# Kernel tuning notes

Hardware: AMD Instinct MI355X
Metric: run time of the kernel (lower is better)

Reference implementation:

```python
import jax, jax.numpy as jnp
import numpy as np

N = 16384
E = 524288
IN_DIM = 512
HID = 256
NCLS = 64


def setup_inputs() -> dict:
    key = jax.random.key(0)
    k1, k2, k3, k4, k5, k6 = jax.random.split(key, 6)
    X = jax.random.normal(k1, (N, IN_DIM), dtype=jnp.float32)
    edge_index = jax.random.randint(k2, (2, E), 0, N, dtype=jnp.int64)
    # torch nn.Linear params: y = x @ W.T + b
    W1 = jax.random.normal(k3, (HID, IN_DIM), dtype=jnp.float32) * (1.0 / np.sqrt(IN_DIM))
    b1 = jax.random.normal(k4, (HID,), dtype=jnp.float32) * 0.01
    W2 = jax.random.normal(k5, (NCLS, HID), dtype=jnp.float32) * (1.0 / np.sqrt(HID))
    b2 = jax.random.normal(k6, (NCLS,), dtype=jnp.float32) * 0.01
    return {"X": X, "edge_index": edge_index, "W1": W1, "b1": b1, "W2": W2, "b2": b2}


def _build_a_hat(edge_index, n):
    # Dense adjacency via scatter-set, exactly as the torch code does.
    A = jnp.zeros((n, n), dtype=jnp.float32)
    A = A.at[edge_index[0], edge_index[1]].set(1.0)
    A = A + A.T
    A = (A > 0).astype(jnp.float32)
    A = A + jnp.eye(n, dtype=jnp.float32)
    # symmetric normalization: D^-1/2 A D^-1/2 (diag matmuls == broadcast)
    deg = A.sum(axis=1)
    dis = jnp.power(deg + 1e-8, -0.5)
    return dis[:, None] * A * dis[None, :]


def reference(X, edge_index, W1, b1, W2, b2):
    n = X.shape[0]
    A_hat = _build_a_hat(edge_index, n)
    H = A_hat @ X                      # [N, in_dim]
    H = H @ W1.T + b1                  # lin1
    H = jax.nn.relu(H)
    # dropout is identity in eval mode
    H = A_hat @ H                      # [N, hidden]
    H = H @ W2.T + b2                  # lin2 -> [N, num_classes]
    return H
```

## Files before the change

### kernel.cpp

```cpp
#include <hip/hip_runtime.h>
#include <stdint.h>

#define N_NODES 16384
#define N_EDGES 524288
#define IN_DIM  512
#define HID     256
#define NCLS    64
#define LSTRIDE 192
#define NBKT    1024
#define SCAP    24
#define NBBLK   256
#define GEMM_BLKS 512

typedef __bf16 bf16x8 __attribute__((ext_vector_type(8)));
typedef float  f32x4  __attribute__((ext_vector_type(4)));

__device__ __forceinline__ unsigned short f2bf(float f) {
    unsigned int u = __float_as_uint(f);
    u += 0x7FFFu + ((u >> 16) & 1u);
    return (unsigned short)(u >> 16);
}
__device__ __forceinline__ float bflo(unsigned int u) { return __uint_as_float(u << 16); }
__device__ __forceinline__ float bfhi(unsigned int u) { return __uint_as_float(u & 0xFFFF0000u); }

__device__ __forceinline__ void bucket_body(
    int blk, const void* __restrict__ ep, unsigned int* __restrict__ cnt,
    unsigned int* __restrict__ gbuf, char* smem) {
    unsigned int* lcnt = (unsigned int*)smem;
    __shared__ int sflag;
    const int tid = threadIdx.x;
    if (tid == 0) {
        const int* p = (const int*)ep;
        int odd = 1;
        for (int k = 0; k < 64; ++k)
            if (p[2 * k + 1] != 0) odd = 0;
        sflag = odd;
    }
    for (int b = tid; b < NBKT; b += 256) lcnt[b] = 0;
    __syncthreads();

    const int e0 = blk * 2048 + tid;
    int s[8], d[8];
    if (sflag) {
        const long long* p = (const long long*)ep;
        #pragma unroll
        for (int q = 0; q < 8; ++q) {
            s[q] = (int)p[e0 + q * 256];
            d[q] = (int)p[N_EDGES + e0 + q * 256];
        }
    } else {
        const int* p = (const int*)ep;
        #pragma unroll
        for (int q = 0; q < 8; ++q) {
            s[q] = p[e0 + q * 256];
            d[q] = p[N_EDGES + e0 + q * 256];
        }
    }
    unsigned int* myslice = gbuf + (size_t)blk * NBKT * SCAP;
    #pragma unroll
    for (int q = 0; q < 8; ++q) {
        int b0 = s[q] >> 4, b1 = d[q] >> 4;
        unsigned int sl0 = atomicAdd(&lcnt[b0], 1u);
        unsigned int sl1 = atomicAdd(&lcnt[b1], 1u);
        if (sl0 < SCAP)
            myslice[b0 * SCAP + sl0] =
                ((unsigned int)(s[q] & 15) << 14) | (unsigned int)d[q];
        if (sl1 < SCAP)
            myslice[b1 * SCAP + sl1] =
                ((unsigned int)(d[q] & 15) << 14) | (unsigned int)s[q];
    }
    __syncthreads();
    unsigned int* mycnt = cnt + (size_t)blk * NBKT;
    for (int b = tid; b < NBKT; b += 256)
        mycnt[b] = min(lcnt[b], (unsigned int)SCAP);
}

__global__ __launch_bounds__(256) void build_csr(
    const unsigned int* __restrict__ cnt, const unsigned int* __restrict__ gbuf,
    float* __restrict__ dis, int* __restrict__ ncnt,
    unsigned short* __restrict__ lists) {
    __shared__ unsigned int bml[16 * 512];
    const int tid = threadIdx.x;
    const int bkt = blockIdx.x;
    const int node0 = bkt * 16;
    #pragma unroll
    for (int q = 0; q < 32; ++q) bml[tid + q * 256] = 0;
    __syncthreads();
    {
        const unsigned int c = cnt[(size_t)tid * NBKT + bkt];
        const unsigned int* sp = gbuf + ((size_t)tid * NBKT + bkt) * SCAP;
        for (unsigned int l = 0; l < c; ++l) {
            unsigned int e = sp[l];
            unsigned int local = e >> 14, nbr = e & 16383u;
            atomicOr(&bml[local * 512 + (nbr >> 5)], 1u << (nbr & 31u));
        }
    }
    __syncthreads();
    const int wid = tid >> 6, lane = tid & 63;
    for (int nn = wid; nn < 16; nn += 4) {
        const int node = node0 + nn;
        const unsigned int* row = bml + nn * 512 + lane * 8;
        unsigned int w[8];
        int c = 0;
        #pragma unroll
        for (int j = 0; j < 8; ++j) { w[j] = row[j]; c += __popc(w[j]); }
        int inc = c;
        #pragma unroll
        for (int dd = 1; dd < 64; dd <<= 1) {
            int t = __shfl_up(inc, dd);
            if (lane >= dd) inc += t;
        }
        int total = __shfl(inc, 63);
        unsigned short* dst = lists + (size_t)node * LSTRIDE + (inc - c);
        int k = 0;
        #pragma unroll
        for (int j = 0; j < 8; ++j) {
            unsigned int bits = w[j];
            int base = (lane * 8 + j) * 32;
            while (bits) {
                int b = __ffs(bits) - 1;
                bits &= bits - 1;
                dst[k++] = (unsigned short)(base + b);
            }
        }
        if (lane == 63) {
            lists[(size_t)node * LSTRIDE + total] = (unsigned short)node;
            ncnt[node] = total + 1;
            dis[node] = 1.0f / sqrtf((float)(total + 1) + 1e-8f);
        }
    }
}

template <bool F32>
__device__ __forceinline__ uint4 ld_chunk(const void* __restrict__ G,
                                          size_t row, int KD, int k0, int s) {
    if constexpr (F32) {
        const float* g = (const float*)G + row * KD + k0 + s * 8;
        float4 v0 = *(const float4*)g;
        float4 v1 = *(const float4*)(g + 4);
        uint4 w;
        w.x = (unsigned int)f2bf(v0.x) | ((unsigned int)f2bf(v0.y) << 16);
        w.y = (unsigned int)f2bf(v0.z) | ((unsigned int)f2bf(v0.w) << 16);
        w.z = (unsigned int)f2bf(v1.x) | ((unsigned int)f2bf(v1.y) << 16);
        w.w = (unsigned int)f2bf(v1.z) | ((unsigned int)f2bf(v1.w) << 16);
        return w;
    } else {
        return *(const uint4*)((const unsigned short*)G + row * KD + k0 + s * 8);
    }
}

template <int BM, int BN, int KD, int ND, bool AF32, bool BF32>
__device__ __forceinline__ void gemm_body(
    int bx, int by, const void* __restrict__ Ag, const void* __restrict__ Bg,
    unsigned short* __restrict__ Cg, const float* __restrict__ dis, char* smem) {
    constexpr int FM = BM / 32, FN = BN / 32;
    constexpr int NK = KD / 64;
    unsigned short* Asm = (unsigned short*)smem;
    unsigned short* Bsm = (unsigned short*)smem + BM * 64;
    const int tid = threadIdx.x;
    const int lane = tid & 63;
    const int wid = tid >> 6;
    const int wm = wid >> 1, wn = wid & 1;
    const int m0 = bx * BM, n0 = by * BN;

    uint4 ra[BM / 32], rb[BN / 32];
    #pragma unroll
    for (int q = 0; q < BM / 32; ++q) {
        int cch = tid + 256 * q, r = cch >> 3, s = cch & 7;
        ra[q] = ld_chunk<AF32>(Ag, (size_t)(m0 + r), KD, 0, s);
    }
    #pragma unroll
    for (int q = 0; q < BN / 32; ++q) {
        int cch = tid + 256 * q, r = cch >> 3, s = cch & 7;
        rb[q] = ld_chunk<BF32>(Bg, (size_t)(n0 + r), KD, 0, s);
    }

    f32x4 acc[FM][FN] = {};

    for (int kt = 0; kt < NK; ++kt) {
        __syncthreads();
        #pragma unroll
        for (int q = 0; q < BM / 32; ++q) {
            int cch = tid + 256 * q, r = cch >> 3, s = cch & 7;
            *(uint4*)((char*)Asm + r * 128 + ((s ^ (r & 7)) << 4)) = ra[q];
        }
        #pragma unroll
        for (int q = 0; q < BN / 32; ++q) {
            int cch = tid + 256 * q, r = cch >> 3, s = cch & 7;
            *(uint4*)((char*)Bsm + r * 128 + ((s ^ (r & 7)) << 4)) = rb[q];
        }
        __syncthreads();
        if (kt + 1 < NK) {
            int k0 = (kt + 1) * 64;
            #pragma unroll
            for (int q = 0; q < BM / 32; ++q) {
                int cch = tid + 256 * q, r = cch >> 3, s = cch & 7;
                ra[q] = ld_chunk<AF32>(Ag, (size_t)(m0 + r), KD, k0, s);
            }
            #pragma unroll
            for (int q = 0; q < BN / 32; ++q) {
                int cch = tid + 256 * q, r = cch >> 3, s = cch & 7;
                rb[q] = ld_chunk<BF32>(Bg, (size_t)(n0 + r), KD, k0, s);
            }
        }
        #pragma unroll
        for (int ks = 0; ks < 2; ++ks) {
            bf16x8 af[FM], bg[FN];
            #pragma unroll
            for (int i = 0; i < FM; ++i) {
                int row = wm * (BM / 2) + i * 16 + (lane & 15);
                int slot = (ks * 4 + (lane >> 4)) ^ (row & 7);
                af[i] = *(const bf16x8*)((const char*)Asm + row * 128 + slot * 16);
            }
            #pragma unroll
            for (int j = 0; j < FN; ++j) {
                int row = wn * (BN / 2) + j * 16 + (lane & 15);
                int slot = (ks * 4 + (lane >> 4)) ^ (row & 7);
                bg[j] = *(const bf16x8*)((const char*)Bsm + row * 128 + slot * 16);
            }
            #pragma unroll
            for (int i = 0; i < FM; ++i)
                #pragma unroll
                for (int j = 0; j < FN; ++j)
                    acc[i][j] = __builtin_amdgcn_mfma_f32_16x16x32_bf16(af[i], bg[j], acc[i][j], 0, 0, 0);
        }
    }

    #pragma unroll
    for (int i = 0; i < FM; ++i) {
        #pragma unroll
        for (int e = 0; e < 4; ++e) {
            int row = m0 + wm * (BM / 2) + i * 16 + ((lane >> 4) << 2) + e;
            float dm = dis ? dis[row] : 1.0f;
            #pragma unroll
            for (int j = 0; j < FN; ++j) {
                int col = n0 + wn * (BN / 2) + j * 16 + (lane & 15);
                Cg[(size_t)row * ND + col] = f2bf(acc[i][j][e] * dm);
            }
        }
    }
}

__global__ __launch_bounds__(256) void bucket_gemm(
    const float* __restrict__ X, const float* __restrict__ W1,
    unsigned short* __restrict__ Y, const void* __restrict__ ep,
    unsigned int* __restrict__ cnt, unsigned int* __restrict__ gbuf) {
    __shared__ __align__(16) char smem[(64 + 128) * 64 * 2];
    if (blockIdx.x < GEMM_BLKS) {
        int gb = blockIdx.x;
        gemm_body<64, 128, IN_DIM, HID, true, true>(
            gb & 255, gb >> 8, X, W1, Y, nullptr, smem);
    } else {
        bucket_body(blockIdx.x - GEMM_BLKS, ep, cnt, gbuf, smem);
    }
}

__global__ __launch_bounds__(256) void gemm2_k(
    const unsigned short* __restrict__ H1, const float* __restrict__ W2,
    unsigned short* __restrict__ Z, const float* __restrict__ dis) {
    __shared__ __align__(16) char smem[(128 + 64) * 64 * 2];
    gemm_body<128, 64, HID, NCLS, false, true>(blockIdx.x, 0, H1, W2, Z, dis, smem);
}

__global__ __launch_bounds__(256) void spmm_hid(
    const int* __restrict__ ncnt, const unsigned short* __restrict__ lists,
    const float* __restrict__ dis, const unsigned short* __restrict__ Yp,
    const float* __restrict__ bias, unsigned int* __restrict__ H1b) {
    const int bid = blockIdx.x;
    const int r = bid & 7;
    const int fh = r >> 2;
    const int wid = threadIdx.x >> 6, lane = threadIdx.x & 63;
    const int i = (bid >> 3) * 16 + (r & 3) * 4 + wid;

    __shared__ unsigned int sl[4][LSTRIDE];
    __shared__ float dl[4][LSTRIDE];
    const int n = min(ncnt[i], LSTRIDE);
    for (int l = lane; l < n; l += 64) {
        int j = lists[(size_t)i * LSTRIDE + l];
        sl[wid][l] = (unsigned int)j << 9;
        dl[wid][l] = dis[j];
    }
    __syncthreads();

    const int hw = lane >> 5, p = lane & 31;
    const char* Ybase = (const char*)Yp + fh * 256 + p * 8;
    float a0 = 0, a1 = 0, a2 = 0, a3 = 0;
    float b0 = 0, b1 = 0, b2 = 0, b3 = 0;
    float c0 = 0, c1 = 0, c2 = 0, c3 = 0;
    float d0 = 0, d1 = 0, d2 = 0, d3 = 0;
    int l = 0;
    for (; l + 8 <= n; l += 8) {
        int i0 = l + hw, i1 = l + 2 + hw, i2 = l + 4 + hw, i3 = l + 6 + hw;
        uint2 u0 = *(const uint2*)(Ybase + sl[wid][i0]);
        uint2 u1 = *(const uint2*)(Ybase + sl[wid][i1]);
        uint2 u2 = *(const uint2*)(Ybase + sl[wid][i2]);
        uint2 u3 = *(const uint2*)(Ybase + sl[wid][i3]);
        float w0 = dl[wid][i0], w1 = dl[wid][i1], w2 = dl[wid][i2], w3 = dl[wid][i3];
        a0 = fmaf(w0, bflo(u0.x), a0); a1 = fmaf(w0, bfhi(u0.x), a1);
        a2 = fmaf(w0, bflo(u0.y), a2); a3 = fmaf(w0, bfhi(u0.y), a3);
        b0 = fmaf(w1, bflo(u1.x), b0); b1 = fmaf(w1, bfhi(u1.x), b1);
        b2 = fmaf(w1, bflo(u1.y), b2); b3 = fmaf(w1, bfhi(u1.y), b3);
        c0 = fmaf(w2, bflo(u2.x), c0); c1 = fmaf(w2, bfhi(u2.x), c1);
        c2 = fmaf(w2, bflo(u2.y), c2); c3 = fmaf(w2, bfhi(u2.y), c3);
        d0 = fmaf(w3, bflo(u3.x), d0); d1 = fmaf(w3, bfhi(u3.x), d1);
        d2 = fmaf(w3, bflo(u3.y), d2); d3 = fmaf(w3, bfhi(u3.y), d3);
    }
    for (; l + hw < n; l += 2) {
        int i0 = l + hw;
        uint2 u = *(const uint2*)(Ybase + sl[wid][i0]);
        float w = dl[wid][i0];
        a0 = fmaf(w, bflo(u.x), a0); a1 = fmaf(w, bfhi(u.x), a1);
        a2 = fmaf(w, bflo(u.y), a2); a3 = fmaf(w, bfhi(u.y), a3);
    }
    a0 += (b0 + c0) + d0; a1 += (b1 + c1) + d1;
    a2 += (b2 + c2) + d2; a3 += (b3 + c3) + d3;
    a0 += __shfl_xor(a0, 32);
    a1 += __shfl_xor(a1, 32);
    a2 += __shfl_xor(a2, 32);
    a3 += __shfl_xor(a3, 32);
    if (hw == 0) {
        float di = dis[i];
        float4 bb = *(const float4*)&bias[fh * 128 + 4 * p];
        float v0 = fmaxf(fmaf(di, a0, bb.x), 0.0f);
        float v1 = fmaxf(fmaf(di, a1, bb.y), 0.0f);
        float v2 = fmaxf(fmaf(di, a2, bb.z), 0.0f);
        float v3 = fmaxf(fmaf(di, a3, bb.w), 0.0f);
        unsigned int olo = (unsigned int)f2bf(v0) | ((unsigned int)f2bf(v1) << 16);
        unsigned int ohi = (unsigned int)f2bf(v2) | ((unsigned int)f2bf(v3) << 16);
        unsigned int* op = &H1b[(size_t)i * 128 + fh * 64 + 2 * p];
        __builtin_nontemporal_store(olo, op);
        __builtin_nontemporal_store(ohi, op + 1);
    }
}

__global__ __launch_bounds__(256) void spmm_out(
    const int* __restrict__ ncnt, const unsigned short* __restrict__ lists,
    const float* __restrict__ dis, const unsigned short* __restrict__ Zp,
    const float* __restrict__ bias, float* __restrict__ out) {
    const int wid = threadIdx.x >> 6, lane = threadIdx.x & 63;
    const int i = blockIdx.x * 4 + wid;
    __shared__ unsigned int sl[4][LSTRIDE];
    const int n = min(ncnt[i], LSTRIDE);
    for (int l = lane; l < n; l += 64)
        sl[wid][l] = (unsigned int)lists[(size_t)i * LSTRIDE + l] << 7;
    __syncthreads();

    const int hw = lane >> 5, p = lane & 31;
    const char* Zbase = (const char*)Zp + p * 4;
    float s0 = 0, s1 = 0, t0 = 0, t1 = 0, q0 = 0, q1 = 0, r0 = 0, r1 = 0;
    int l = 0;
    for (; l + 8 <= n; l += 8) {
        unsigned int ua = *(const unsigned int*)(Zbase + sl[wid][l + hw]);
        unsigned int ub = *(const unsigned int*)(Zbase + sl[wid][l + 2 + hw]);
        unsigned int uc = *(const unsigned int*)(Zbase + sl[wid][l + 4 + hw]);
        unsigned int ud = *(const unsigned int*)(Zbase + sl[wid][l + 6 + hw]);
        s0 += bflo(ua); s1 += bfhi(ua);
        t0 += bflo(ub); t1 += bfhi(ub);
        q0 += bflo(uc); q1 += bfhi(uc);
        r0 += bflo(ud); r1 += bfhi(ud);
    }
    for (; l + hw < n; l += 2) {
        unsigned int u = *(const unsigned int*)(Zbase + sl[wid][l + hw]);
        s0 += bflo(u); s1 += bfhi(u);
    }
    s0 += (t0 + q0) + r0; s1 += (t1 + q1) + r1;
    s0 += __shfl_xor(s0, 32);
    s1 += __shfl_xor(s1, 32);
    if (hw == 0) {
        float di = dis[i];
        __builtin_nontemporal_store(fmaf(di, s0, bias[2 * p]), &out[(size_t)i * 64 + 2 * p]);
        __builtin_nontemporal_store(fmaf(di, s1, bias[2 * p + 1]), &out[(size_t)i * 64 + 2 * p + 1]);
    }
}

extern "C" void kernel_launch(void* const* d_in, const int* in_sizes, int n_in,
                              void* d_out, int out_size, void* d_ws, size_t ws_size,
                              hipStream_t stream) {
    const float* X  = (const float*)d_in[0];
    const void*  EI = d_in[1];
    const float* W1 = (const float*)d_in[2];
    const float* b1 = (const float*)d_in[3];
    const float* W2 = (const float*)d_in[4];
    const float* b2 = (const float*)d_in[5];
    float* out = (float*)d_out;

    char* ws = (char*)d_ws;
    char* p = ws;
    unsigned int* cnt  = (unsigned int*)p;       p += (size_t)NBBLK * NBKT * 4;
    unsigned int* gbuf = (unsigned int*)p;       p += (size_t)NBBLK * NBKT * SCAP * 4;
    float* dis = (float*)p;                      p += (size_t)N_NODES * 4;
    int* ncnt = (int*)p;                         p += (size_t)N_NODES * 4;
    unsigned short* lists = (unsigned short*)p;  p += (size_t)N_NODES * LSTRIDE * 2;
    unsigned short* Y   = (unsigned short*)p;    p += (size_t)N_NODES * HID * 2;
    unsigned int* H1b   = (unsigned int*)p;      p += (size_t)N_NODES * HID * 2;
    unsigned short* Z   = (unsigned short*)p;    p += (size_t)N_NODES * NCLS * 2;

    bucket_gemm<<<GEMM_BLKS + NBBLK, 256, 0, stream>>>(X, W1, Y, EI, cnt, gbuf);
    build_csr<<<NBKT, 256, 0, stream>>>(cnt, gbuf, dis, ncnt, lists);
    spmm_hid<<<2 * N_NODES / 4, 256, 0, stream>>>(ncnt, lists, dis, Y, b1, H1b);
    gemm2_k<<<N_NODES / 128, 256, 0, stream>>>((const unsigned short*)H1b, W2, Z, dis);
    spmm_out<<<N_NODES / 4, 256, 0, stream>>>(ncnt, lists, dis, Z, b2, out);
}
```

Baseline: 115.2 us.

## Widen SpMM gathers to 16-byte loads, enlarge GEMM1 tile, transpose bucket counts

The two SpMM kernels now gather neighbour rows with 16-byte vector loads and spread more neighbours across lane groups, using shuffle reductions at the end. In spmm_hid each neighbour's weight and offset are packed into one uint2 in shared memory. The first GEMM switches to 128x128 tiles with half as many blocks. The bucket count array is transposed so build_csr reads it coalesced. The aim is fewer memory transactions and less gather latency, at the cost of more registers, more shuffle work and less GEMM parallelism.

```diff
diff --git a/kernel.cpp b/kernel.cpp
--- a/kernel.cpp
+++ b/kernel.cpp
@@ -10,10 +10,11 @@
 #define NBKT    1024
 #define SCAP    24
 #define NBBLK   256
-#define GEMM_BLKS 512
+#define GEMM_BLKS 256
 
 typedef __bf16 bf16x8 __attribute__((ext_vector_type(8)));
 typedef float  f32x4  __attribute__((ext_vector_type(4)));
+typedef unsigned int u32x4 __attribute__((ext_vector_type(4)));
 
 __device__ __forceinline__ unsigned short f2bf(float f) {
     unsigned int u = __float_as_uint(f);
@@ -70,9 +71,8 @@
                 ((unsigned int)(d[q] & 15) << 14) | (unsigned int)s[q];
     }
     __syncthreads();
-    unsigned int* mycnt = cnt + (size_t)blk * NBKT;
     for (int b = tid; b < NBKT; b += 256)
-        mycnt[b] = min(lcnt[b], (unsigned int)SCAP);
+        cnt[(size_t)b * NBBLK + blk] = min(lcnt[b], (unsigned int)SCAP);
 }
 
 __global__ __launch_bounds__(256) void build_csr(
@@ -87,7 +87,7 @@
     for (int q = 0; q < 32; ++q) bml[tid + q * 256] = 0;
     __syncthreads();
     {
-        const unsigned int c = cnt[(size_t)tid * NBKT + bkt];
+        const unsigned int c = cnt[(size_t)bkt * NBBLK + tid];
         const unsigned int* sp = gbuf + ((size_t)tid * NBKT + bkt) * SCAP;
         for (unsigned int l = 0; l < c; ++l) {
             unsigned int e = sp[l];
@@ -245,11 +245,11 @@
     const float* __restrict__ X, const float* __restrict__ W1,
     unsigned short* __restrict__ Y, const void* __restrict__ ep,
     unsigned int* __restrict__ cnt, unsigned int* __restrict__ gbuf) {
-    __shared__ __align__(16) char smem[(64 + 128) * 64 * 2];
+    __shared__ __align__(16) char smem[(128 + 128) * 64 * 2];
     if (blockIdx.x < GEMM_BLKS) {
         int gb = blockIdx.x;
-        gemm_body<64, 128, IN_DIM, HID, true, true>(
-            gb & 255, gb >> 8, X, W1, Y, nullptr, smem);
+        gemm_body<128, 128, IN_DIM, HID, true, true>(
+            gb & 127, gb >> 7, X, W1, Y, nullptr, smem);
     } else {
         bucket_body(blockIdx.x - GEMM_BLKS, ep, cnt, gbuf, smem);
     }
@@ -265,71 +265,78 @@
 __global__ __launch_bounds__(256) void spmm_hid(
     const int* __restrict__ ncnt, const unsigned short* __restrict__ lists,
     const float* __restrict__ dis, const unsigned short* __restrict__ Yp,
-    const float* __restrict__ bias, unsigned int* __restrict__ H1b) {
+    const float* __restrict__ bias, unsigned short* __restrict__ H1) {
     const int bid = blockIdx.x;
     const int r = bid & 7;
     const int fh = r >> 2;
     const int wid = threadIdx.x >> 6, lane = threadIdx.x & 63;
     const int i = (bid >> 3) * 16 + (r & 3) * 4 + wid;
 
-    __shared__ unsigned int sl[4][LSTRIDE];
-    __shared__ float dl[4][LSTRIDE];
+    __shared__ uint2 sld[4][LSTRIDE];
     const int n = min(ncnt[i], LSTRIDE);
     for (int l = lane; l < n; l += 64) {
         int j = lists[(size_t)i * LSTRIDE + l];
-        sl[wid][l] = (unsigned int)j << 9;
-        dl[wid][l] = dis[j];
-    }
-    __syncthreads();
-
-    const int hw = lane >> 5, p = lane & 31;
-    const char* Ybase = (const char*)Yp + fh * 256 + p * 8;
-    float a0 = 0, a1 = 0, a2 = 0, a3 = 0;
-    float b0 = 0, b1 = 0, b2 = 0, b3 = 0;
-    float c0 = 0, c1 = 0, c2 = 0, c3 = 0;
-    float d0 = 0, d1 = 0, d2 = 0, d3 = 0;
+        uint2 m;
+        m.x = __float_as_uint(dis[j]);
+        m.y = (unsigned int)j << 9;
+        sld[wid][l] = m;
+    }
+    __syncthreads();
+
+    const int qw = lane >> 4, p = lane & 15;
+    const char* Ybase = (const char*)Yp + fh * 256 + p * 16;
+    float acc[8] = {}, acc2[8] = {};
     int l = 0;
     for (; l + 8 <= n; l += 8) {
-        int i0 = l + hw, i1 = l + 2 + hw, i2 = l + 4 + hw, i3 = l + 6 + hw;
-        uint2 u0 = *(const uint2*)(Ybase + sl[wid][i0]);
-        uint2 u1 = *(const uint2*)(Ybase + sl[wid][i1]);
-        uint2 u2 = *(const uint2*)(Ybase + sl[wid][i2]);
-        uint2 u3 = *(const uint2*)(Ybase + sl[wid][i3]);
-        float w0 = dl[wid][i0], w1 = dl[wid][i1], w2 = dl[wid][i2], w3 = dl[wid][i3];
-        a0 = fmaf(w0, bflo(u0.x), a0); a1 = fmaf(w0, bfhi(u0.x), a1);
-        a2 = fmaf(w0, bflo(u0.y), a2); a3 = fmaf(w0, bfhi(u0.y), a3);
-        b0 = fmaf(w1, bflo(u1.x), b0); b1 = fmaf(w1, bfhi(u1.x), b1);
-        b2 = fmaf(w1, bflo(u1.y), b2); b3 = fmaf(w1, bfhi(u1.y), b3);
-        c0 = fmaf(w2, bflo(u2.x), c0); c1 = fmaf(w2, bfhi(u2.x), c1);
-        c2 = fmaf(w2, bflo(u2.y), c2); c3 = fmaf(w2, bfhi(u2.y), c3);
-        d0 = fmaf(w3, bflo(u3.x), d0); d1 = fmaf(w3, bfhi(u3.x), d1);
-        d2 = fmaf(w3, bflo(u3.y), d2); d3 = fmaf(w3, bfhi(u3.y), d3);
-    }
-    for (; l + hw < n; l += 2) {
-        int i0 = l + hw;
-        uint2 u = *(const uint2*)(Ybase + sl[wid][i0]);
-        float w = dl[wid][i0];
-        a0 = fmaf(w, bflo(u.x), a0); a1 = fmaf(w, bfhi(u.x), a1);
-        a2 = fmaf(w, bflo(u.y), a2); a3 = fmaf(w, bfhi(u.y), a3);
-    }
-    a0 += (b0 + c0) + d0; a1 += (b1 + c1) + d1;
-    a2 += (b2 + c2) + d2; a3 += (b3 + c3) + d3;
-    a0 += __shfl_xor(a0, 32);
-    a1 += __shfl_xor(a1, 32);
-    a2 += __shfl_xor(a2, 32);
-    a3 += __shfl_xor(a3, 32);
-    if (hw == 0) {
+        uint2 m0 = sld[wid][l + qw];
+        uint2 m1 = sld[wid][l + 4 + qw];
+        uint4 u0 = *(const uint4*)(Ybase + m0.y);
+        uint4 u1 = *(const uint4*)(Ybase + m1.y);
+        float w0 = __uint_as_float(m0.x), w1 = __uint_as_float(m1.x);
+        acc[0] = fmaf(w0, bflo(u0.x), acc[0]); acc[1] = fmaf(w0, bfhi(u0.x), acc[1]);
+        acc[2] = fmaf(w0, bflo(u0.y), acc[2]); acc[3] = fmaf(w0, bfhi(u0.y), acc[3]);
+        acc[4] = fmaf(w0, bflo(u0.z), acc[4]); acc[5] = fmaf(w0, bfhi(u0.z), acc[5]);
+        acc[6] = fmaf(w0, bflo(u0.w), acc[6]); acc[7] = fmaf(w0, bfhi(u0.w), acc[7]);
+        acc2[0] = fmaf(w1, bflo(u1.x), acc2[0]); acc2[1] = fmaf(w1, bfhi(u1.x), acc2[1]);
+        acc2[2] = fmaf(w1, bflo(u1.y), acc2[2]); acc2[3] = fmaf(w1, bfhi(u1.y), acc2[3]);
+        acc2[4] = fmaf(w1, bflo(u1.z), acc2[4]); acc2[5] = fmaf(w1, bfhi(u1.z), acc2[5]);
+        acc2[6] = fmaf(w1, bflo(u1.w), acc2[6]); acc2[7] = fmaf(w1, bfhi(u1.w), acc2[7]);
+    }
+    for (; l < n; l += 4) {
+        if (l + qw < n) {
+            uint2 m = sld[wid][l + qw];
+            uint4 u = *(const uint4*)(Ybase + m.y);
+            float w = __uint_as_float(m.x);
+            acc[0] = fmaf(w, bflo(u.x), acc[0]); acc[1] = fmaf(w, bfhi(u.x), acc[1]);
+            acc[2] = fmaf(w, bflo(u.y), acc[2]); acc[3] = fmaf(w, bfhi(u.y), acc[3]);
+            acc[4] = fmaf(w, bflo(u.z), acc[4]); acc[5] = fmaf(w, bfhi(u.z), acc[5]);
+            acc[6] = fmaf(w, bflo(u.w), acc[6]); acc[7] = fmaf(w, bfhi(u.w), acc[7]);
+        }
+    }
+    #pragma unroll
+    for (int k = 0; k < 8; ++k) {
+        acc[k] += acc2[k];
+        acc[k] += __shfl_xor(acc[k], 16);
+        acc[k] += __shfl_xor(acc[k], 32);
+    }
+    if (qw == 0) {
         float di = dis[i];
-        float4 bb = *(const float4*)&bias[fh * 128 + 4 * p];
-        float v0 = fmaxf(fmaf(di, a0, bb.x), 0.0f);
-        float v1 = fmaxf(fmaf(di, a1, bb.y), 0.0f);
-        float v2 = fmaxf(fmaf(di, a2, bb.z), 0.0f);
-        float v3 = fmaxf(fmaf(di, a3, bb.w), 0.0f);
-        unsigned int olo = (unsigned int)f2bf(v0) | ((unsigned int)f2bf(v1) << 16);
-        unsigned int ohi = (unsigned int)f2bf(v2) | ((unsigned int)f2bf(v3) << 16);
-        unsigned int* op = &H1b[(size_t)i * 128 + fh * 64 + 2 * p];
-        __builtin_nontemporal_store(olo, op);
-        __builtin_nontemporal_store(ohi, op + 1);
+        float4 b0 = *(const float4*)&bias[fh * 128 + p * 8];
+        float4 b1 = *(const float4*)&bias[fh * 128 + p * 8 + 4];
+        float v0 = fmaxf(fmaf(di, acc[0], b0.x), 0.0f);
+        float v1 = fmaxf(fmaf(di, acc[1], b0.y), 0.0f);
+        float v2 = fmaxf(fmaf(di, acc[2], b0.z), 0.0f);
+        float v3 = fmaxf(fmaf(di, acc[3], b0.w), 0.0f);
+        float v4 = fmaxf(fmaf(di, acc[4], b1.x), 0.0f);
+        float v5 = fmaxf(fmaf(di, acc[5], b1.y), 0.0f);
+        float v6 = fmaxf(fmaf(di, acc[6], b1.z), 0.0f);
+        float v7 = fmaxf(fmaf(di, acc[7], b1.w), 0.0f);
+        u32x4 o;
+        o.x = (unsigned int)f2bf(v0) | ((unsigned int)f2bf(v1) << 16);
+        o.y = (unsigned int)f2bf(v2) | ((unsigned int)f2bf(v3) << 16);
+        o.z = (unsigned int)f2bf(v4) | ((unsigned int)f2bf(v5) << 16);
+        o.w = (unsigned int)f2bf(v6) | ((unsigned int)f2bf(v7) << 16);
+        __builtin_nontemporal_store(o, (u32x4*)&H1[(size_t)i * 256 + fh * 128 + p * 8]);
     }
 }
 
@@ -345,31 +352,50 @@
         sl[wid][l] = (unsigned int)lists[(size_t)i * LSTRIDE + l] << 7;
     __syncthreads();
 
-    const int hw = lane >> 5, p = lane & 31;
-    const char* Zbase = (const char*)Zp + p * 4;
-    float s0 = 0, s1 = 0, t0 = 0, t1 = 0, q0 = 0, q1 = 0, r0 = 0, r1 = 0;
+    const int g = lane >> 3, p = lane & 7;
+    const char* Zbase = (const char*)Zp + p * 16;
+    float acc[8] = {}, acc2[8] = {};
     int l = 0;
-    for (; l + 8 <= n; l += 8) {
-        unsigned int ua = *(const unsigned int*)(Zbase + sl[wid][l + hw]);
-        unsigned int ub = *(const unsigned int*)(Zbase + sl[wid][l + 2 + hw]);
-        unsigned int uc = *(const unsigned int*)(Zbase + sl[wid][l + 4 + hw]);
-        unsigned int ud = *(const unsigned int*)(Zbase + sl[wid][l + 6 + hw]);
-        s0 += bflo(ua); s1 += bfhi(ua);
-        t0 += bflo(ub); t1 += bfhi(ub);
-        q0 += bflo(uc); q1 += bfhi(uc);
-        r0 += bflo(ud); r1 += bfhi(ud);
-    }
-    for (; l + hw < n; l += 2) {
-        unsigned int u = *(const unsigned int*)(Zbase + sl[wid][l + hw]);
-        s0 += bflo(u); s1 += bfhi(u);
-    }
-    s0 += (t0 + q0) + r0; s1 += (t1 + q1) + r1;
-    s0 += __shfl_xor(s0, 32);
-    s1 += __shfl_xor(s1, 32);
-    if (hw == 0) {
+    for (; l + 16 <= n; l += 16) {
+        uint4 u0 = *(const uint4*)(Zbase + sl[wid][l + g]);
+        uint4 u1 = *(const uint4*)(Zbase + sl[wid][l + 8 + g]);
+        acc[0] += bflo(u0.x); acc[1] += bfhi(u0.x);
+        acc[2] += bflo(u0.y); acc[3] += bfhi(u0.y);
+        acc[4] += bflo(u0.z); acc[5] += bfhi(u0.z);
+        acc[6] += bflo(u0.w); acc[7] += bfhi(u0.w);
+        acc2[0] += bflo(u1.x); acc2[1] += bfhi(u1.x);
+        acc2[2] += bflo(u1.y); acc2[3] += bfhi(u1.y);
+        acc2[4] += bflo(u1.z); acc2[5] += bfhi(u1.z);
+        acc2[6] += bflo(u1.w); acc2[7] += bfhi(u1.w);
+    }
+    for (; l < n; l += 8) {
+        if (l + g < n) {
+            uint4 u = *(const uint4*)(Zbase + sl[wid][l + g]);
+            acc[0] += bflo(u.x); acc[1] += bfhi(u.x);
+            acc[2] += bflo(u.y); acc[3] += bfhi(u.y);
+            acc[4] += bflo(u.z); acc[5] += bfhi(u.z);
+            acc[6] += bflo(u.w); acc[7] += bfhi(u.w);
+        }
+    }
+    #pragma unroll
+    for (int k = 0; k < 8; ++k) {
+        acc[k] += acc2[k];
+        acc[k] += __shfl_xor(acc[k], 8);
+        acc[k] += __shfl_xor(acc[k], 16);
+        acc[k] += __shfl_xor(acc[k], 32);
+    }
+    if (lane < 8) {
         float di = dis[i];
-        __builtin_nontemporal_store(fmaf(di, s0, bias[2 * p]), &out[(size_t)i * 64 + 2 * p]);
-        __builtin_nontemporal_store(fmaf(di, s1, bias[2 * p + 1]), &out[(size_t)i * 64 + 2 * p + 1]);
+        float4 b0 = *(const float4*)&bias[p * 8];
+        float4 b1 = *(const float4*)&bias[p * 8 + 4];
+        f32x4 o0, o1;
+        o0.x = fmaf(di, acc[0], b0.x); o0.y = fmaf(di, acc[1], b0.y);
+        o0.z = fmaf(di, acc[2], b0.z); o0.w = fmaf(di, acc[3], b0.w);
+        o1.x = fmaf(di, acc[4], b1.x); o1.y = fmaf(di, acc[5], b1.y);
+        o1.z = fmaf(di, acc[6], b1.z); o1.w = fmaf(di, acc[7], b1.w);
+        float* op = &out[(size_t)i * 64 + p * 8];
+        __builtin_nontemporal_store(o0, (f32x4*)op);
+        __builtin_nontemporal_store(o1, (f32x4*)(op + 4));
     }
 }
 
@@ -392,12 +418,12 @@
     int* ncnt = (int*)p;                         p += (size_t)N_NODES * 4;
     unsigned short* lists = (unsigned short*)p;  p += (size_t)N_NODES * LSTRIDE * 2;
     unsigned short* Y   = (unsigned short*)p;    p += (size_t)N_NODES * HID * 2;
-    unsigned int* H1b   = (unsigned int*)p;      p += (size_t)N_NODES * HID * 2;
+    unsigned short* H1  = (unsigned short*)p;    p += (size_t)N_NODES * HID * 2;
     unsigned short* Z   = (unsigned short*)p;    p += (size_t)N_NODES * NCLS * 2;
 
     bucket_gemm<<<GEMM_BLKS + NBBLK, 256, 0, stream>>>(X, W1, Y, EI, cnt, gbuf);
     build_csr<<<NBKT, 256, 0, stream>>>(cnt, gbuf, dis, ncnt, lists);
-    spmm_hid<<<2 * N_NODES / 4, 256, 0, stream>>>(ncnt, lists, dis, Y, b1, H1b);
-    gemm2_k<<<N_NODES / 128, 256, 0, stream>>>((const unsigned short*)H1b, W2, Z, dis);
+    spmm_hid<<<2 * N_NODES / 4, 256, 0, stream>>>(ncnt, lists, dis, Y, b1, H1);
+    gemm2_k<<<N_NODES / 128, 256, 0, stream>>>(H1, W2, Z, dis);
     spmm_out<<<N_NODES / 4, 256, 0, stream>>>(ncnt, lists, dis, Z, b2, out);
 }
```

Result: faster. 107.6 us (-6.6%).
